# Performance work log

Hardware: AMD Instinct MI355X
Metric: run time of the kernel (lower is better)

The kernel has to match this reference:

```python
import jax, jax.numpy as jnp
import numpy as np

B, N, D = 8, 4096, 256

def setup_inputs() -> dict:
    key = jax.random.key(0)
    k1, k2, k3 = jax.random.split(key, 3)
    x = jax.random.normal(k1, (B, N, D), dtype=jnp.float32)
    # torch nn.Linear(D, 3D): weight [3D, D], bias [3D]
    W_qkv = jax.random.normal(k2, (3 * D, D), dtype=jnp.float32) * (1.0 / np.sqrt(D))
    b_qkv = jax.random.normal(k3, (3 * D,), dtype=jnp.float32) * 0.01
    return {"x": x, "W_qkv": W_qkv, "b_qkv": b_qkv}

def reference(x, W_qkv, b_qkv):
    Dm = x.shape[-1]
    qkv = jnp.einsum('bnd,ed->bne', x, W_qkv) + b_qkv  # [B,N,3D]
    q, k, v = jnp.split(qkv, 3, axis=-1)
    scale = 1.0 / jnp.sqrt(jnp.asarray(Dm, dtype=x.dtype))
    scores = jnp.einsum('bnd,bmd->bnm', q, k) * scale  # [B,N,N]
    attn = jax.nn.softmax(scores, axis=-1)
    return jnp.einsum('bnm,bmd->bnd', attn, v)
```

## Files before the change

### kernel.cpp

```cpp
#include <hip/hip_runtime.h>
#include <hip/hip_bf16.h>


typedef __attribute__((ext_vector_type(8))) short short8;
typedef __attribute__((ext_vector_type(4))) float f32x4;
typedef __attribute__((ext_vector_type(16))) float f32x16;

#define MFMA16(A, B, C) __builtin_amdgcn_mfma_f32_16x16x32_bf16(A, B, C, 0, 0, 0)
#define MFMA32(A, B, C) __builtin_amdgcn_mfma_f32_32x32x16_bf16(A, B, C, 0, 0, 0)

__device__ __forceinline__ unsigned short f2bf(float f) {
  union { float f; unsigned u; } v; v.f = f;
  unsigned r = v.u + 0x7FFFu + ((v.u >> 16) & 1u);
  return (unsigned short)(r >> 16);
}

__device__ __forceinline__ ushort4 pack4(float4 v) {
  ushort4 r;
  r.x = f2bf(v.x); r.y = f2bf(v.y); r.z = f2bf(v.z); r.w = f2bf(v.w);
  return r;
}

__device__ __forceinline__ unsigned packbf2(float a, float b) {
  union { __hip_bfloat162 b2; unsigned u; } cv;
  cv.b2 = __float22bfloat162_rn(make_float2(a, b));
  return cv.u;
}

__device__ __forceinline__ void gload_lds16(const void* g, void* l) {
  __builtin_amdgcn_global_load_lds(
      (const __attribute__((address_space(1))) void*)g,
      (__attribute__((address_space(3))) void*)l, 16, 0, 0);
}

template <int MODE>
__global__ __launch_bounds__(256)
void proj_kernel(const float* __restrict__ A, const float* __restrict__ Bm,
                 const float* __restrict__ bias,
                 unsigned short* __restrict__ Qs, unsigned short* __restrict__ Kb,
                 unsigned short* __restrict__ VT) {
  __shared__ __align__(16) unsigned short as_[2][128 * 64];
  __shared__ __align__(16) unsigned short bs_[2][128 * 64];

  const int tid = threadIdx.x;
  const int wid = tid >> 6, lane = tid & 63, l15 = lane & 15, lhi = lane >> 4;
  int m0, n0;
  if (MODE == 0) { m0 = blockIdx.y * 128; n0 = blockIdx.x * 128; }
  else           { m0 = blockIdx.x * 128; n0 = blockIdx.y * 128; }
  const float* Arow = A + (size_t)m0 * 256;
  const float* Brow = Bm + (size_t)n0 * 256;

  const int srow = tid >> 4;
  const int c4 = tid & 15;
  float4 ra[8], rb[8];

  auto loadslice = [&](int kc) {
#pragma unroll
    for (int i = 0; i < 8; ++i) {
      int row = i * 16 + srow;
      ra[i] = *(const float4*)(Arow + (size_t)row * 256 + kc * 64 + c4 * 4);
      rb[i] = *(const float4*)(Brow + (size_t)row * 256 + kc * 64 + c4 * 4);
    }
  };
  auto writeslice = [&](int buf) {
#pragma unroll
    for (int i = 0; i < 8; ++i) {
      int row = i * 16 + srow;
      int g = c4 >> 1, half = c4 & 1;
      int off = row * 64 + ((g ^ (row & 7)) << 3) + half * 4;
      *(ushort4*)&as_[buf][off] = pack4(ra[i]);
      *(ushort4*)&bs_[buf][off] = pack4(rb[i]);
    }
  };

  f32x4 acc[2][8];
#pragma unroll
  for (int mt = 0; mt < 2; ++mt)
#pragma unroll
    for (int nt = 0; nt < 8; ++nt) acc[mt][nt] = (f32x4){0.f, 0.f, 0.f, 0.f};

  loadslice(0);
  writeslice(0);
  int cur = 0;
  for (int kc = 0; kc < 4; ++kc) {
    __syncthreads();
    if (kc < 3) loadslice(kc + 1);
#pragma unroll
    for (int ks = 0; ks < 2; ++ks) {
      short8 af[2];
#pragma unroll
      for (int mt = 0; mt < 2; ++mt) {
        int row = wid * 32 + mt * 16 + l15;
        int g = ks * 4 + lhi;
        af[mt] = *(const short8*)&as_[cur][row * 64 + ((g ^ (row & 7)) << 3)];
      }
#pragma unroll
      for (int nt = 0; nt < 8; ++nt) {
        int row = nt * 16 + l15;
        int g = ks * 4 + lhi;
        short8 bf = *(const short8*)&bs_[cur][row * 64 + ((g ^ (row & 7)) << 3)];
        acc[0][nt] = MFMA16(af[0], bf, acc[0][nt]);
        acc[1][nt] = MFMA16(af[1], bf, acc[1][nt]);
      }
    }
    if (kc < 3) writeslice(cur ^ 1);
    cur ^= 1;
  }

  const float QSC = 0.0901684400555602f;
#pragma unroll
  for (int nt = 0; nt < 8; ++nt) {
    if (MODE == 0) {
      int e = n0 + nt * 16 + l15;
      float bv = bias[e];
#pragma unroll
      for (int mt = 0; mt < 2; ++mt)
#pragma unroll
        for (int r = 0; r < 4; ++r) {
          int tok = m0 + wid * 32 + mt * 16 + lhi * 4 + r;
          float val = acc[mt][nt][r] + bv;
          if (e < 256) Qs[(size_t)tok * 256 + e] = f2bf(val * QSC);
          else         Kb[(size_t)tok * 256 + (e - 256)] = f2bf(val);
        }
    } else {
      int tok = n0 + nt * 16 + l15;
      int bb = tok >> 12, n = tok & 4095;
      int t4 = n & 15;
      int flip = ((t4 >> 2) ^ (t4 >> 3)) & 1;
      int n2 = (n & ~15) | (t4 ^ (flip ? 12 : 0));
#pragma unroll
      for (int mt = 0; mt < 2; ++mt)
#pragma unroll
        for (int r = 0; r < 4; ++r) {
          int d = m0 + wid * 32 + mt * 16 + lhi * 4 + r;
          float val = acc[mt][nt][r] + bias[512 + d];
          VT[(size_t)bb * (256 * 4096) + (size_t)d * 4096 + n2] = f2bf(val);
        }
    }
  }
}

__global__ __launch_bounds__(512, 2)
void attn_kernel(const unsigned short* __restrict__ Qs,
                 const unsigned short* __restrict__ Kb,
                 const unsigned short* __restrict__ VT,
                 float* __restrict__ out) {
  __shared__ __align__(16) unsigned short lds_kv[2][2][16384];
  __shared__ float2 lds_ml[8][32];

  const int tid = threadIdx.x;
  const int wid = tid >> 6, lane = tid & 63, l31 = lane & 31, h = lane >> 5;
  const int hv = wid >> 2;
  const int qg = wid & 3;
  const int tid_h = tid & 255;
  const int blk = blockIdx.x;
  const int b = blk & 7;
  const int qblk = blk >> 3;
  const int q0 = qblk * 128 + qg * 32;

  const unsigned short* qp = Qs + ((size_t)b * 4096 + q0 + l31) * 256 + h * 8;
  short8 qf[16];
#pragma unroll
  for (int ks = 0; ks < 16; ++ks) qf[ks] = *(const short8*)(qp + ks * 16);

  f32x16 acco[8];
#pragma unroll
  for (int dt = 0; dt < 8; ++dt)
#pragma unroll
    for (int j = 0; j < 16; ++j) acco[dt][j] = 0.f;
  float m = -1e30f, lsum = 0.f;

  const unsigned short* kbase = Kb + (size_t)b * 4096 * 256;
  const unsigned short* vtb   = VT + (size_t)b * 256 * 4096;

  auto stage = [&](int it, int buf) {
    const int kv0 = hv * 2048 + it * 32;
    unsigned short* kbuf = &lds_kv[hv][buf][0];
    unsigned short* vbuf = &lds_kv[hv][buf][8192];
    const unsigned short* ksrc = kbase + (size_t)kv0 * 256;
#pragma unroll
    for (int i = 0; i < 4; ++i) {
      int g = i * 256 + tid_h;
      int row = g >> 5, cp = g & 31;
      int sg = (row << 5) | (cp ^ (row & 7));
      gload_lds16(ksrc + sg * 8, kbuf + (i * 256 + (qg << 6)) * 8);
    }
#pragma unroll
    for (int i = 0; i < 4; ++i) {
      int g = i * 256 + tid_h;
      int d = g >> 2, cp = g & 3;
      int sc = cp ^ ((d >> 1) & 3);
      gload_lds16(vtb + (size_t)d * 4096 + kv0 + sc * 8,
                  vbuf + (i * 256 + (qg << 6)) * 8);
    }
  };

  stage(0, 0);
  int cur = 0;
  for (int it = 0; it < 64; ++it) {
    __syncthreads();
    if (it < 63) stage(it + 1, cur ^ 1);
    const unsigned short* kb = &lds_kv[hv][cur][0];
    const unsigned short* vb = &lds_kv[hv][cur][8192];

    f32x16 s0;
#pragma unroll
    for (int j = 0; j < 16; ++j) s0[j] = 0.f;
    __builtin_amdgcn_s_setprio(1);
#pragma unroll
    for (int ks = 0; ks < 16; ++ks) {
      const short8 kf =
          *(const short8*)&kb[l31 * 256 + (((2 * ks + h) ^ (l31 & 7)) << 3)];
      s0 = MFMA32(kf, qf[ks], s0);
    }
    __builtin_amdgcn_s_setprio(0);

    float mx = s0[0];
#pragma unroll
    for (int r = 1; r < 16; ++r) mx = fmaxf(mx, s0[r]);
    mx = fmaxf(mx, __shfl_xor(mx, 32));
    const float mo = m;
    const float mn = (mx > mo + 4.f) ? mx : mo;
    const float al = __builtin_amdgcn_exp2f(mo - mn);
    m = mn;
    if (__any(mn != mo)) {
      float alq[16];
#pragma unroll
      for (int r = 0; r < 16; ++r)
        alq[r] = __shfl(al, (r & 3) + 8 * (r >> 2) + 4 * h, 64);
#pragma unroll
      for (int dt = 0; dt < 8; ++dt)
#pragma unroll
        for (int r = 0; r < 16; ++r) acco[dt][r] *= alq[r];
    }

#pragma unroll
    for (int r = 0; r < 8; ++r) s0[r] = __builtin_amdgcn_exp2f(s0[r] - mn);
    short8 pf0;
    {
      union { unsigned u[4]; short8 v; } a0;
#pragma unroll
      for (int k2 = 0; k2 < 4; ++k2)
        a0.u[k2] = packbf2(s0[2 * k2], s0[2 * k2 + 1]);
      pf0 = a0.v;
    }
    __builtin_amdgcn_s_setprio(1);
#pragma unroll
    for (int dt = 0; dt < 8; ++dt) {
      const int d = dt * 32 + l31;
      const short8 vf =
          *(const short8*)&vb[d * 32 + ((h ^ ((l31 >> 1) & 3)) << 3)];
      acco[dt] = MFMA32(pf0, vf, acco[dt]);
    }
    __builtin_amdgcn_s_setprio(0);
#pragma unroll
    for (int r = 8; r < 16; ++r) s0[r] = __builtin_amdgcn_exp2f(s0[r] - mn);
    short8 pf1;
    {
      union { unsigned u[4]; short8 v; } a1;
#pragma unroll
      for (int k2 = 0; k2 < 4; ++k2)
        a1.u[k2] = packbf2(s0[8 + 2 * k2], s0[9 + 2 * k2]);
      pf1 = a1.v;
    }
    __builtin_amdgcn_s_setprio(1);
#pragma unroll
    for (int dt = 0; dt < 8; ++dt) {
      const int d = dt * 32 + l31;
      const short8 vf =
          *(const short8*)&vb[d * 32 + (((2 + h) ^ ((l31 >> 1) & 3)) << 3)];
      acco[dt] = MFMA32(pf1, vf, acco[dt]);
    }
    __builtin_amdgcn_s_setprio(0);

    float rs = 0.f;
#pragma unroll
    for (int r = 0; r < 16; ++r) rs += s0[r];
    rs += __shfl_xor(rs, 32);
    lsum = lsum * al + rs;
    cur ^= 1;
  }

  __syncthreads();
  if (lane < 32) lds_ml[wid][lane] = make_float2(m, lsum);
  float* o_base = (float*)&lds_kv[0][0][0];
  if (hv == 1) {
    float* o = o_base + qg * 8192;
#pragma unroll
    for (int dt = 0; dt < 8; ++dt)
#pragma unroll
      for (int r = 0; r < 16; ++r) {
        int qp2 = (r & 3) + 8 * (r >> 2) + 4 * h;
        o[qp2 * 256 + dt * 32 + l31] = acco[dt][r];
      }
  }
  __syncthreads();
  if (hv == 0) {
    float* o = o_base + qg * 8192;
    float* orow = out + ((size_t)b * 4096 + q0) * 256;
#pragma unroll
    for (int r = 0; r < 16; ++r) {
      int qp2 = (r & 3) + 8 * (r >> 2) + 4 * h;
      float2 s_own = lds_ml[wid][qp2];
      float2 s_par = lds_ml[wid + 4][qp2];
      float mM = fmaxf(s_own.x, s_par.x);
      float w0 = __builtin_amdgcn_exp2f(s_own.x - mM);
      float w1 = __builtin_amdgcn_exp2f(s_par.x - mM);
      float inv = 1.f / (w0 * s_own.y + w1 * s_par.y);
#pragma unroll
      for (int dt = 0; dt < 8; ++dt) {
        float val = (acco[dt][r] * w0 + o[qp2 * 256 + dt * 32 + l31] * w1) * inv;
        orow[(size_t)qp2 * 256 + dt * 32 + l31] = val;
      }
    }
  }
}

extern "C" void kernel_launch(void* const* d_in, const int* in_sizes, int n_in,
                              void* d_out, int out_size, void* d_ws, size_t ws_size,
                              hipStream_t stream) {
  const float* x    = (const float*)d_in[0];
  const float* W    = (const float*)d_in[1];
  const float* bias = (const float*)d_in[2];
  float* out = (float*)d_out;

  char* ws = (char*)d_ws;
  unsigned short* Qs = (unsigned short*)(ws);
  unsigned short* Kb = (unsigned short*)(ws + (size_t)16 * 1024 * 1024);
  unsigned short* VT = (unsigned short*)(ws + (size_t)32 * 1024 * 1024);

  proj_kernel<0><<<dim3(4, 256), 256, 0, stream>>>(x, W, bias, Qs, Kb, VT);
  proj_kernel<1><<<dim3(2, 256), 256, 0, stream>>>(W + 512 * 256, x, bias, Qs, Kb, VT);
  attn_kernel<<<256, 512, 0, stream>>>(Qs, Kb, VT, out);
}
```

Before: 243.8 us.

## Split attention KV range across separate blocks with a global merge kernel

Replaces the fused kernel, which split the KV range between two wave groups inside one 512-thread block and merged through LDS, with independent 256-thread blocks. Each block handles half of the KV sequence and writes unnormalized partial outputs plus running max and sum to workspace. A separate merge kernel then combines them. The old fused kernel is kept as a fallback for small workspaces, and its loop is reordered to compute all exponentials before the PV MFMAs, with the setprio hints removed. The split path adds about 32 MB of extra fp32 global traffic and one more launch, in exchange for smaller blocks and possibly better scheduling.

```diff
diff --git a/kernel.cpp b/kernel.cpp
--- a/kernel.cpp
+++ b/kernel.cpp
@@ -140,11 +140,182 @@
   }
 }
 
+__global__ __launch_bounds__(256, 2)
+void attn_split(const unsigned short* __restrict__ Qs,
+                const unsigned short* __restrict__ Kb,
+                const unsigned short* __restrict__ VT,
+                float* __restrict__ out, float* __restrict__ O1,
+                float2* __restrict__ ML) {
+  __shared__ __align__(16) unsigned short lds_kv[2][16384];
+
+  const int tid = threadIdx.x;
+  const int wid = tid >> 6, lane = tid & 63, l31 = lane & 31, h = lane >> 5;
+  const int blk = blockIdx.x;
+  const int b = blk & 7;
+  const int hh = (blk >> 3) & 1;
+  const int qblk = blk >> 4;
+  const int q0 = qblk * 128 + wid * 32;
+
+  const unsigned short* qp = Qs + ((size_t)b * 4096 + q0 + l31) * 256 + h * 8;
+  short8 qf[16];
+#pragma unroll
+  for (int ks = 0; ks < 16; ++ks) qf[ks] = *(const short8*)(qp + ks * 16);
+
+  f32x16 acco[8];
+#pragma unroll
+  for (int dt = 0; dt < 8; ++dt)
+#pragma unroll
+    for (int j = 0; j < 16; ++j) acco[dt][j] = 0.f;
+  float m = -1e30f, lsum = 0.f;
+
+  const unsigned short* kbase = Kb + (size_t)b * 4096 * 256;
+  const unsigned short* vtb   = VT + (size_t)b * 256 * 4096;
+
+  auto stage = [&](int it, int buf) {
+    const int kv0 = hh * 2048 + it * 32;
+    unsigned short* kbuf = &lds_kv[buf][0];
+    unsigned short* vbuf = &lds_kv[buf][8192];
+    const unsigned short* ksrc = kbase + (size_t)kv0 * 256;
+#pragma unroll
+    for (int i = 0; i < 4; ++i) {
+      int g = i * 256 + tid;
+      int row = g >> 5, cp = g & 31;
+      int sg = (row << 5) | (cp ^ (row & 7));
+      gload_lds16(ksrc + sg * 8, kbuf + (i * 256 + (wid << 6)) * 8);
+    }
+#pragma unroll
+    for (int i = 0; i < 4; ++i) {
+      int g = i * 256 + tid;
+      int d = g >> 2, cp = g & 3;
+      int sc = cp ^ ((d >> 1) & 3);
+      gload_lds16(vtb + (size_t)d * 4096 + kv0 + sc * 8,
+                  vbuf + (i * 256 + (wid << 6)) * 8);
+    }
+  };
+
+  stage(0, 0);
+  int cur = 0;
+  for (int it = 0; it < 64; ++it) {
+    __syncthreads();
+    if (it < 63) stage(it + 1, cur ^ 1);
+    const unsigned short* kb = &lds_kv[cur][0];
+    const unsigned short* vb = &lds_kv[cur][8192];
+
+    f32x16 s0;
+#pragma unroll
+    for (int j = 0; j < 16; ++j) s0[j] = 0.f;
+    __builtin_amdgcn_s_setprio(1);
+#pragma unroll
+    for (int ks = 0; ks < 16; ++ks) {
+      const short8 kf =
+          *(const short8*)&kb[l31 * 256 + (((2 * ks + h) ^ (l31 & 7)) << 3)];
+      s0 = MFMA32(kf, qf[ks], s0);
+    }
+    __builtin_amdgcn_s_setprio(0);
+
+    float mx = s0[0];
+#pragma unroll
+    for (int r = 1; r < 16; ++r) mx = fmaxf(mx, s0[r]);
+    mx = fmaxf(mx, __shfl_xor(mx, 32));
+    const float mo = m;
+    const float mn = (mx > mo + 4.f) ? mx : mo;
+    const float al = __builtin_amdgcn_exp2f(mo - mn);
+    m = mn;
+    if (__any(mn != mo)) {
+      float alq[16];
+#pragma unroll
+      for (int r = 0; r < 16; ++r)
+        alq[r] = __shfl(al, (r & 3) + 8 * (r >> 2) + 4 * h, 64);
+#pragma unroll
+      for (int dt = 0; dt < 8; ++dt)
+#pragma unroll
+        for (int r = 0; r < 16; ++r) acco[dt][r] *= alq[r];
+    }
+
+#pragma unroll
+    for (int r = 0; r < 8; ++r) s0[r] = __builtin_amdgcn_exp2f(s0[r] - mn);
+    short8 pf0;
+    {
+      union { unsigned u[4]; short8 v; } a0;
+#pragma unroll
+      for (int k2 = 0; k2 < 4; ++k2)
+        a0.u[k2] = packbf2(s0[2 * k2], s0[2 * k2 + 1]);
+      pf0 = a0.v;
+    }
+    __builtin_amdgcn_s_setprio(1);
+#pragma unroll
+    for (int dt = 0; dt < 8; ++dt) {
+      const int d = dt * 32 + l31;
+      const short8 vf =
+          *(const short8*)&vb[d * 32 + ((h ^ ((l31 >> 1) & 3)) << 3)];
+      acco[dt] = MFMA32(pf0, vf, acco[dt]);
+    }
+    __builtin_amdgcn_s_setprio(0);
+#pragma unroll
+    for (int r = 8; r < 16; ++r) s0[r] = __builtin_amdgcn_exp2f(s0[r] - mn);
+    short8 pf1;
+    {
+      union { unsigned u[4]; short8 v; } a1;
+#pragma unroll
+      for (int k2 = 0; k2 < 4; ++k2)
+        a1.u[k2] = packbf2(s0[8 + 2 * k2], s0[9 + 2 * k2]);
+      pf1 = a1.v;
+    }
+    __builtin_amdgcn_s_setprio(1);
+#pragma unroll
+    for (int dt = 0; dt < 8; ++dt) {
+      const int d = dt * 32 + l31;
+      const short8 vf =
+          *(const short8*)&vb[d * 32 + (((2 + h) ^ ((l31 >> 1) & 3)) << 3)];
+      acco[dt] = MFMA32(pf1, vf, acco[dt]);
+    }
+    __builtin_amdgcn_s_setprio(0);
+
+    float rs = 0.f;
+#pragma unroll
+    for (int r = 0; r < 16; ++r) rs += s0[r];
+    rs += __shfl_xor(rs, 32);
+    lsum = lsum * al + rs;
+    cur ^= 1;
+  }
+
+  float* op = (hh ? O1 : out) + ((size_t)b * 4096 + q0) * 256;
+#pragma unroll
+  for (int dt = 0; dt < 8; ++dt)
+#pragma unroll
+    for (int r = 0; r < 16; ++r) {
+      int qp2 = (r & 3) + 8 * (r >> 2) + 4 * h;
+      op[(size_t)qp2 * 256 + dt * 32 + l31] = acco[dt][r];
+    }
+  if (lane < 32)
+    ML[hh * 32768 + (size_t)b * 4096 + q0 + lane] = make_float2(m, lsum);
+}
+
+__global__ __launch_bounds__(256)
+void merge_kernel(float* __restrict__ out, const float* __restrict__ O1,
+                  const float2* __restrict__ ML) {
+  const int i4 = blockIdx.x * 256 + threadIdx.x;
+  const int row = i4 >> 6;
+  const float2 s0 = ML[row], s1 = ML[32768 + row];
+  const float mM = fmaxf(s0.x, s1.x);
+  const float w0 = __builtin_amdgcn_exp2f(s0.x - mM);
+  const float w1 = __builtin_amdgcn_exp2f(s1.x - mM);
+  const float inv = 1.f / (w0 * s0.y + w1 * s1.y);
+  const float4 a = ((const float4*)out)[i4];
+  const float4 c = ((const float4*)O1)[i4];
+  float4 r;
+  r.x = (a.x * w0 + c.x * w1) * inv;
+  r.y = (a.y * w0 + c.y * w1) * inv;
+  r.z = (a.z * w0 + c.z * w1) * inv;
+  r.w = (a.w * w0 + c.w * w1) * inv;
+  ((float4*)out)[i4] = r;
+}
+
 __global__ __launch_bounds__(512, 2)
-void attn_kernel(const unsigned short* __restrict__ Qs,
-                 const unsigned short* __restrict__ Kb,
-                 const unsigned short* __restrict__ VT,
-                 float* __restrict__ out) {
+void attn_fused(const unsigned short* __restrict__ Qs,
+                const unsigned short* __restrict__ Kb,
+                const unsigned short* __restrict__ VT,
+                float* __restrict__ out) {
   __shared__ __align__(16) unsigned short lds_kv[2][2][16384];
   __shared__ float2 lds_ml[8][32];
 
@@ -206,14 +377,12 @@
     f32x16 s0;
 #pragma unroll
     for (int j = 0; j < 16; ++j) s0[j] = 0.f;
-    __builtin_amdgcn_s_setprio(1);
 #pragma unroll
     for (int ks = 0; ks < 16; ++ks) {
       const short8 kf =
           *(const short8*)&kb[l31 * 256 + (((2 * ks + h) ^ (l31 & 7)) << 3)];
       s0 = MFMA32(kf, qf[ks], s0);
     }
-    __builtin_amdgcn_s_setprio(0);
 
     float mx = s0[0];
 #pragma unroll
@@ -234,50 +403,35 @@
         for (int r = 0; r < 16; ++r) acco[dt][r] *= alq[r];
     }
 
-#pragma unroll
-    for (int r = 0; r < 8; ++r) s0[r] = __builtin_amdgcn_exp2f(s0[r] - mn);
-    short8 pf0;
-    {
-      union { unsigned u[4]; short8 v; } a0;
-#pragma unroll
-      for (int k2 = 0; k2 < 4; ++k2)
-        a0.u[k2] = packbf2(s0[2 * k2], s0[2 * k2 + 1]);
-      pf0 = a0.v;
-    }
-    __builtin_amdgcn_s_setprio(1);
-#pragma unroll
-    for (int dt = 0; dt < 8; ++dt) {
-      const int d = dt * 32 + l31;
-      const short8 vf =
-          *(const short8*)&vb[d * 32 + ((h ^ ((l31 >> 1) & 3)) << 3)];
-      acco[dt] = MFMA32(pf0, vf, acco[dt]);
-    }
-    __builtin_amdgcn_s_setprio(0);
-#pragma unroll
-    for (int r = 8; r < 16; ++r) s0[r] = __builtin_amdgcn_exp2f(s0[r] - mn);
-    short8 pf1;
-    {
-      union { unsigned u[4]; short8 v; } a1;
-#pragma unroll
-      for (int k2 = 0; k2 < 4; ++k2)
-        a1.u[k2] = packbf2(s0[8 + 2 * k2], s0[9 + 2 * k2]);
-      pf1 = a1.v;
-    }
-    __builtin_amdgcn_s_setprio(1);
-#pragma unroll
-    for (int dt = 0; dt < 8; ++dt) {
-      const int d = dt * 32 + l31;
-      const short8 vf =
-          *(const short8*)&vb[d * 32 + (((2 + h) ^ ((l31 >> 1) & 3)) << 3)];
-      acco[dt] = MFMA32(pf1, vf, acco[dt]);
-    }
-    __builtin_amdgcn_s_setprio(0);
-
     float rs = 0.f;
 #pragma unroll
-    for (int r = 0; r < 16; ++r) rs += s0[r];
+    for (int r = 0; r < 16; ++r) {
+      s0[r] = __builtin_amdgcn_exp2f(s0[r] - mn);
+      rs += s0[r];
+    }
     rs += __shfl_xor(rs, 32);
     lsum = lsum * al + rs;
+
+    short8 pf[2];
+    {
+      union { unsigned u[4]; short8 v; } a0, a1;
+#pragma unroll
+      for (int k2 = 0; k2 < 4; ++k2) {
+        a0.u[k2] = packbf2(s0[2 * k2], s0[2 * k2 + 1]);
+        a1.u[k2] = packbf2(s0[8 + 2 * k2], s0[9 + 2 * k2]);
+      }
+      pf[0] = a0.v; pf[1] = a1.v;
+    }
+#pragma unroll
+    for (int ks = 0; ks < 2; ++ks) {
+#pragma unroll
+      for (int dt = 0; dt < 8; ++dt) {
+        const int d = dt * 32 + l31;
+        const short8 vf = *(const short8*)
+            &vb[d * 32 + (((2 * ks + h) ^ ((l31 >> 1) & 3)) << 3)];
+        acco[dt] = MFMA32(pf[ks], vf, acco[dt]);
+      }
+    }
     cur ^= 1;
   }
 
@@ -328,8 +482,17 @@
   unsigned short* Qs = (unsigned short*)(ws);
   unsigned short* Kb = (unsigned short*)(ws + (size_t)16 * 1024 * 1024);
   unsigned short* VT = (unsigned short*)(ws + (size_t)32 * 1024 * 1024);
+  float*          O1 = (float*)(ws + (size_t)48 * 1024 * 1024);
+  float2*         ML = (float2*)(ws + (size_t)80 * 1024 * 1024);
 
   proj_kernel<0><<<dim3(4, 256), 256, 0, stream>>>(x, W, bias, Qs, Kb, VT);
   proj_kernel<1><<<dim3(2, 256), 256, 0, stream>>>(W + 512 * 256, x, bias, Qs, Kb, VT);
-  attn_kernel<<<256, 512, 0, stream>>>(Qs, Kb, VT, out);
-}
+
+  const size_t NEED = (size_t)81 * 1024 * 1024;
+  if (ws_size >= NEED) {
+    attn_split<<<512, 256, 0, stream>>>(Qs, Kb, VT, out, O1, ML);
+    merge_kernel<<<8192, 256, 0, stream>>>(out, O1, ML);
+  } else {
+    attn_fused<<<256, 512, 0, stream>>>(Qs, Kb, VT, out);
+  }
+}
```

After: 243.7 us. About the same (-0.1%).

## Split attention KV across four waves per 32-query block with per-wave staging

Applied to the files above, without the earlier changes.

Each attention block now handles 32 queries with 4 waves, and each wave processes a quarter of the KV sequence. Each wave stages its own K/V tiles into private LDS with explicit waitcnt instead of block-wide barriers, preloads K and V fragments into registers before the MFMAs, and issues the next tile's loads after the QK step. Cross-half reductions use permlane32_swap instead of shuffles. A 4-way softmax merge runs at the end. The goal is to remove __syncthreads from the inner loop and raise grid parallelism, at the cost of a single LDS buffer per wave (weaker load overlap), each Q fragment being loaded by four times as many blocks, and a heavier final merge.

```diff
diff --git a/kernel.cpp b/kernel.cpp
--- a/kernel.cpp
+++ b/kernel.cpp
@@ -5,6 +5,7 @@
 typedef __attribute__((ext_vector_type(8))) short short8;
 typedef __attribute__((ext_vector_type(4))) float f32x4;
 typedef __attribute__((ext_vector_type(16))) float f32x16;
+typedef __attribute__((ext_vector_type(2))) unsigned uint2v;
 
 #define MFMA16(A, B, C) __builtin_amdgcn_mfma_f32_16x16x32_bf16(A, B, C, 0, 0, 0)
 #define MFMA32(A, B, C) __builtin_amdgcn_mfma_f32_32x32x16_bf16(A, B, C, 0, 0, 0)
@@ -31,6 +32,17 @@
   __builtin_amdgcn_global_load_lds(
       (const __attribute__((address_space(1))) void*)g,
       (__attribute__((address_space(3))) void*)l, 16, 0, 0);
+}
+
+__device__ __forceinline__ float xhalf_max(float x) {
+  uint2v r = __builtin_amdgcn_permlane32_swap(
+      __float_as_uint(x), __float_as_uint(x), false, false);
+  return fmaxf(__uint_as_float(r.x), __uint_as_float(r.y));
+}
+__device__ __forceinline__ float xhalf_sum(float x) {
+  uint2v r = __builtin_amdgcn_permlane32_swap(
+      __float_as_uint(x), __float_as_uint(x), false, false);
+  return __uint_as_float(r.x) + __uint_as_float(r.y);
 }
 
 template <int MODE>
@@ -140,23 +152,20 @@
   }
 }
 
-__global__ __launch_bounds__(512, 2)
+__global__ __launch_bounds__(256, 1)
 void attn_kernel(const unsigned short* __restrict__ Qs,
                  const unsigned short* __restrict__ Kb,
                  const unsigned short* __restrict__ VT,
                  float* __restrict__ out) {
-  __shared__ __align__(16) unsigned short lds_kv[2][2][16384];
-  __shared__ float2 lds_ml[8][32];
+  __shared__ __align__(16) unsigned short lds_kv[4][16384];
+  __shared__ float2 mlb[4][32];
 
   const int tid = threadIdx.x;
   const int wid = tid >> 6, lane = tid & 63, l31 = lane & 31, h = lane >> 5;
-  const int hv = wid >> 2;
-  const int qg = wid & 3;
-  const int tid_h = tid & 255;
   const int blk = blockIdx.x;
   const int b = blk & 7;
   const int qblk = blk >> 3;
-  const int q0 = qblk * 128 + qg * 32;
+  const int q0 = qblk * 32;
 
   const unsigned short* qp = Qs + ((size_t)b * 4096 + q0 + l31) * 256 + h * 8;
   short8 qf[16];
@@ -172,53 +181,65 @@
 
   const unsigned short* kbase = Kb + (size_t)b * 4096 * 256;
   const unsigned short* vtb   = VT + (size_t)b * 256 * 4096;
-
-  auto stage = [&](int it, int buf) {
-    const int kv0 = hv * 2048 + it * 32;
-    unsigned short* kbuf = &lds_kv[hv][buf][0];
-    unsigned short* vbuf = &lds_kv[hv][buf][8192];
+  unsigned short* kbuf = &lds_kv[wid][0];
+  unsigned short* vbuf = &lds_kv[wid][8192];
+
+  auto stage = [&](int it) {
+    const int kv0 = wid * 1024 + it * 32;
     const unsigned short* ksrc = kbase + (size_t)kv0 * 256;
 #pragma unroll
-    for (int i = 0; i < 4; ++i) {
-      int g = i * 256 + tid_h;
+    for (int i = 0; i < 16; ++i) {
+      int g = i * 64 + lane;
       int row = g >> 5, cp = g & 31;
       int sg = (row << 5) | (cp ^ (row & 7));
-      gload_lds16(ksrc + sg * 8, kbuf + (i * 256 + (qg << 6)) * 8);
-    }
-#pragma unroll
-    for (int i = 0; i < 4; ++i) {
-      int g = i * 256 + tid_h;
+      gload_lds16(ksrc + sg * 8, kbuf + (size_t)(i * 64) * 8);
+    }
+#pragma unroll
+    for (int i = 0; i < 16; ++i) {
+      int g = i * 64 + lane;
       int d = g >> 2, cp = g & 3;
       int sc = cp ^ ((d >> 1) & 3);
       gload_lds16(vtb + (size_t)d * 4096 + kv0 + sc * 8,
-                  vbuf + (i * 256 + (qg << 6)) * 8);
+                  vbuf + (size_t)(i * 64) * 8);
     }
   };
 
-  stage(0, 0);
-  int cur = 0;
-  for (int it = 0; it < 64; ++it) {
-    __syncthreads();
-    if (it < 63) stage(it + 1, cur ^ 1);
-    const unsigned short* kb = &lds_kv[hv][cur][0];
-    const unsigned short* vb = &lds_kv[hv][cur][8192];
+  stage(0);
+  for (int it = 0; it < 32; ++it) {
+    asm volatile("s_waitcnt vmcnt(0)" ::: "memory");
+    __builtin_amdgcn_sched_barrier(0);
+
+    short8 kreg[16];
+#pragma unroll
+    for (int ks = 0; ks < 16; ++ks)
+      kreg[ks] =
+          *(const short8*)&kbuf[l31 * 256 + (((2 * ks + h) ^ (l31 & 7)) << 3)];
+    short8 vreg[2][8];
+#pragma unroll
+    for (int kt = 0; kt < 2; ++kt)
+#pragma unroll
+      for (int dt = 0; dt < 8; ++dt) {
+        const int d = dt * 32 + l31;
+        vreg[kt][dt] = *(const short8*)
+            &vbuf[d * 32 + (((2 * kt + h) ^ ((l31 >> 1) & 3)) << 3)];
+      }
 
     f32x16 s0;
 #pragma unroll
     for (int j = 0; j < 16; ++j) s0[j] = 0.f;
     __builtin_amdgcn_s_setprio(1);
 #pragma unroll
-    for (int ks = 0; ks < 16; ++ks) {
-      const short8 kf =
-          *(const short8*)&kb[l31 * 256 + (((2 * ks + h) ^ (l31 & 7)) << 3)];
-      s0 = MFMA32(kf, qf[ks], s0);
-    }
+    for (int ks = 0; ks < 16; ++ks) s0 = MFMA32(kreg[ks], qf[ks], s0);
     __builtin_amdgcn_s_setprio(0);
 
+    asm volatile("s_waitcnt lgkmcnt(0)" ::: "memory");
+    __builtin_amdgcn_sched_barrier(0);
+    if (it < 31) stage(it + 1);
+
     float mx = s0[0];
 #pragma unroll
     for (int r = 1; r < 16; ++r) mx = fmaxf(mx, s0[r]);
-    mx = fmaxf(mx, __shfl_xor(mx, 32));
+    mx = xhalf_max(mx);
     const float mo = m;
     const float mn = (mx > mo + 4.f) ? mx : mo;
     const float al = __builtin_amdgcn_exp2f(mo - mn);
@@ -246,12 +267,7 @@
     }
     __builtin_amdgcn_s_setprio(1);
 #pragma unroll
-    for (int dt = 0; dt < 8; ++dt) {
-      const int d = dt * 32 + l31;
-      const short8 vf =
-          *(const short8*)&vb[d * 32 + ((h ^ ((l31 >> 1) & 3)) << 3)];
-      acco[dt] = MFMA32(pf0, vf, acco[dt]);
-    }
+    for (int dt = 0; dt < 8; ++dt) acco[dt] = MFMA32(pf0, vreg[0][dt], acco[dt]);
     __builtin_amdgcn_s_setprio(0);
 #pragma unroll
     for (int r = 8; r < 16; ++r) s0[r] = __builtin_amdgcn_exp2f(s0[r] - mn);
@@ -265,52 +281,49 @@
     }
     __builtin_amdgcn_s_setprio(1);
 #pragma unroll
-    for (int dt = 0; dt < 8; ++dt) {
-      const int d = dt * 32 + l31;
-      const short8 vf =
-          *(const short8*)&vb[d * 32 + (((2 + h) ^ ((l31 >> 1) & 3)) << 3)];
-      acco[dt] = MFMA32(pf1, vf, acco[dt]);
-    }
+    for (int dt = 0; dt < 8; ++dt) acco[dt] = MFMA32(pf1, vreg[1][dt], acco[dt]);
     __builtin_amdgcn_s_setprio(0);
 
     float rs = 0.f;
 #pragma unroll
     for (int r = 0; r < 16; ++r) rs += s0[r];
-    rs += __shfl_xor(rs, 32);
+    rs = xhalf_sum(rs);
     lsum = lsum * al + rs;
-    cur ^= 1;
   }
 
   __syncthreads();
-  if (lane < 32) lds_ml[wid][lane] = make_float2(m, lsum);
-  float* o_base = (float*)&lds_kv[0][0][0];
-  if (hv == 1) {
-    float* o = o_base + qg * 8192;
+  float* fbuf = (float*)&lds_kv[0][0];
+  if (wid > 0) {
+    float* mb = fbuf + (size_t)(wid - 1) * 8192;
 #pragma unroll
     for (int dt = 0; dt < 8; ++dt)
 #pragma unroll
       for (int r = 0; r < 16; ++r) {
         int qp2 = (r & 3) + 8 * (r >> 2) + 4 * h;
-        o[qp2 * 256 + dt * 32 + l31] = acco[dt][r];
-      }
-  }
+        mb[qp2 * 256 + dt * 32 + l31] = acco[dt][r];
+      }
+  }
+  if (lane < 32) mlb[wid][lane] = make_float2(m, lsum);
   __syncthreads();
-  if (hv == 0) {
-    float* o = o_base + qg * 8192;
+  if (wid == 0) {
     float* orow = out + ((size_t)b * 4096 + q0) * 256;
 #pragma unroll
     for (int r = 0; r < 16; ++r) {
       int qp2 = (r & 3) + 8 * (r >> 2) + 4 * h;
-      float2 s_own = lds_ml[wid][qp2];
-      float2 s_par = lds_ml[wid + 4][qp2];
-      float mM = fmaxf(s_own.x, s_par.x);
-      float w0 = __builtin_amdgcn_exp2f(s_own.x - mM);
-      float w1 = __builtin_amdgcn_exp2f(s_par.x - mM);
-      float inv = 1.f / (w0 * s_own.y + w1 * s_par.y);
+      float2 s1 = mlb[0][qp2], s2 = mlb[1][qp2];
+      float2 s3 = mlb[2][qp2], s4 = mlb[3][qp2];
+      float mM = fmaxf(fmaxf(s1.x, s2.x), fmaxf(s3.x, s4.x));
+      float w1 = __builtin_amdgcn_exp2f(s1.x - mM);
+      float w2 = __builtin_amdgcn_exp2f(s2.x - mM);
+      float w3 = __builtin_amdgcn_exp2f(s3.x - mM);
+      float w4 = __builtin_amdgcn_exp2f(s4.x - mM);
+      float inv = 1.f / (w1 * s1.y + w2 * s2.y + w3 * s3.y + w4 * s4.y);
 #pragma unroll
       for (int dt = 0; dt < 8; ++dt) {
-        float val = (acco[dt][r] * w0 + o[qp2 * 256 + dt * 32 + l31] * w1) * inv;
-        orow[(size_t)qp2 * 256 + dt * 32 + l31] = val;
+        int off = qp2 * 256 + dt * 32 + l31;
+        float v = acco[dt][r] * w1 + fbuf[off] * w2 +
+                  fbuf[8192 + off] * w3 + fbuf[16384 + off] * w4;
+        orow[off] = v * inv;
       }
     }
   }
@@ -331,5 +344,5 @@
 
   proj_kernel<0><<<dim3(4, 256), 256, 0, stream>>>(x, W, bias, Qs, Kb, VT);
   proj_kernel<1><<<dim3(2, 256), 256, 0, stream>>>(W + 512 * 256, x, bias, Qs, Kb, VT);
-  attn_kernel<<<256, 512, 0, stream>>>(Qs, Kb, VT, out);
-}
+  attn_kernel<<<1024, 256, 0, stream>>>(Qs, Kb, VT, out);
+}
```

Result: slower. 472.5 us (+93.8%).
